# Kernel optimization log

Measured on AMD Instinct MI355X. Metric: run time of the kernel, lower is better.

## Reference

```python
import jax, jax.numpy as jnp
import numpy as np

N = 8192        # nodes
D_IN = 512      # input features
H = 256         # hidden (GAT out_features)
D_OUT = 16      # output classes
K = 16          # num clusters/classes
LRELU_SLOPE = 0.2
MASK_FILL = -9e15
EDGE_P = 0.002  # sparsity of random adjacency


def setup_inputs() -> dict:
    key = jax.random.key(0)
    k1, k2, k3, k4, k5, k6 = jax.random.split(key, 6)
    x = jax.random.normal(k1, (N, D_IN), dtype=jnp.float32)
    # binary adjacency with self loops (module only tests adj > 0; support reused as propagation matrix)
    adj = (jax.random.uniform(k2, (N, N)) < EDGE_P).astype(jnp.float32)
    adj = jnp.maximum(adj, jnp.eye(N, dtype=jnp.float32))
    C_a = jax.random.normal(k3, (K, H), dtype=jnp.float32)
    # learned parameters (xavier-ish scale)
    W = jax.random.normal(k4, (D_IN, H), dtype=jnp.float32) * (1.414 * (2.0 / (D_IN + H)) ** 0.5)
    a = jax.random.normal(k5, (2 * H, 1), dtype=jnp.float32) * (1.414 * (2.0 / (2 * H + 1)) ** 0.5)
    W_gcn = jax.random.normal(k6, (H, D_OUT), dtype=jnp.float32)
    return {"x": x, "adj": adj, "C_a": C_a, "W": W, "a": a, "W_gcn": W_gcn}


def _clust_score(Z, C):
    # score[n,k] = exp(-||Z_n - C_k||) normalized over k (beta = 1)
    d = jnp.sqrt(((Z[:, None, :] - C[None, :, :]) ** 2).sum(-1))  # [N,K]
    s = jnp.exp(-d) + 1e-10
    return s / s.sum(axis=1, keepdims=True)


def reference(x, adj, C_a, W, a, W_gcn):
    h = W.shape[1]
    # --- GAT layer ---
    Wh = x @ W                                   # [N,H]
    Wh1 = Wh @ a[:h, :]                          # [N,1]
    Wh2 = Wh @ a[h:, :]                          # [N,1]
    e = jax.nn.leaky_relu(Wh1 + Wh2.T, LRELU_SLOPE)   # [N,N]
    att = jax.nn.softmax(jnp.where(adj > 0, e, MASK_FILL), axis=1)
    Z_0 = att @ Wh                               # h_prime, [N,H]
    gatoutput = jax.nn.elu(Z_0)
    # --- cluster score on detached Z_0 (update=False path) ---
    score = _clust_score(jax.lax.stop_gradient(Z_0), C_a)
    # --- GCN layer (B_1 = I, so Z_1 = F_1) ---
    F_1 = jax.nn.relu(adj @ (gatoutput @ W_gcn))  # [N,D_OUT]
    output = F_1
    Z_1 = F_1
    return (output, Z_1, Z_0, score)
```

## Files before the change

kernel.cpp:

```cpp
#include <hip/hip_runtime.h>
#include <hip/hip_bf16.h>

#define N_NODES 8192
#define D_IN    512
#define H       256
#define D_OUT   16
#define K_CL    16
#define MAXN    96

#define OUT_OFF 0
#define Z1_OFF  131072
#define Z0_OFF  262144
#define SC_OFF  2359296

typedef unsigned int   u32;
typedef unsigned short u16;
typedef __attribute__((ext_vector_type(8))) short bf16x8;
typedef __attribute__((ext_vector_type(4))) float f32x4;

__device__ __forceinline__ float load_in(const void* p, int bf, size_t idx) {
    if (bf) { u32 w = ((const u16*)p)[idx]; return __uint_as_float(w << 16); }
    return ((const float*)p)[idx];
}
__device__ __forceinline__ void store_out(void* p, int bf, size_t idx, float v) {
    if (bf) ((__hip_bfloat16*)p)[idx] = __float2bfloat16(v);
    else    ((float*)p)[idx] = v;
}
__device__ __forceinline__ int detect_bf(const void* adj) {
    return ((const u32*)adj)[0] != 0x3F800000u;
}
__device__ __forceinline__ float bf2f(u32 h) { return __uint_as_float(h << 16); }

__global__ void k_prep_small(const void* av, const void* C_a, const void* Wgcn,
                             const void* __restrict__ adj,
                             float* a_f, float* Ca_f, float* Wg_f) {
    int bf = detect_bf(adj);
    int i = blockIdx.x * 256 + threadIdx.x;
    if (i < 512)        a_f[i]         = load_in(av,   bf, i);
    else if (i < 4608)  Ca_f[i - 512]  = load_in(C_a,  bf, i - 512);
    else if (i < 8704)  Wg_f[i - 4608] = load_in(Wgcn, bf, i - 4608);
}

__global__ __launch_bounds__(256) void k_prep_wt(
    const void* __restrict__ wraw, const void* __restrict__ adj,
    u16* __restrict__ Wt)
{
    int bf = detect_bf(adj);
    __shared__ float tile[64][65];
    int b = blockIdx.x;
    int k0 = (b >> 2) * 64, h0 = (b & 3) * 64;
    int tid = threadIdx.x;
    int hh = tid & 63, kk = tid >> 6;
    #pragma unroll
    for (int p = 0; p < 16; p++) {
        int k = kk * 16 + p;
        tile[k][hh] = load_in(wraw, bf, (size_t)(k0 + k) * H + h0 + hh);
    }
    __syncthreads();
    int kc = tid & 63, hr = tid >> 6;
    #pragma unroll
    for (int p = 0; p < 16; p++) {
        int h = hr * 16 + p;
        __hip_bfloat16 bb = __float2bfloat16(tile[kc][h]);
        Wt[(size_t)(h0 + h) * D_IN + k0 + kc] = *(u16*)&bb;
    }
}

__global__ __launch_bounds__(256) void k_gemm_wh(
    const void* __restrict__ xraw, const void* __restrict__ wraw,
    const u16* __restrict__ Wt, const void* __restrict__ adj,
    float* __restrict__ Wh, u16* __restrict__ Whb)
{
    int bf = detect_bf(adj);
    __shared__ float xs[32][68];
    __shared__ float ws_[32][68];
    int tid = threadIdx.x;
    int bm = blockIdx.x >> 2, bn = blockIdx.x & 3;
    int m0 = bm * 64, n0 = bn * 64;

    if (bf) {
        int wave = tid >> 6, lane = tid & 63;
        int wr = wave >> 1, wc = wave & 1;
        int r0 = m0 + wr * 32, c0 = n0 + wc * 32;
        int lr = lane & 15, lk = lane >> 4;
        const u16* xp = (const u16*)xraw;
        const u16* a0p = xp + (size_t)(r0 + lr)      * D_IN + lk * 8;
        const u16* a1p = xp + (size_t)(r0 + 16 + lr) * D_IN + lk * 8;
        const u16* b0p = Wt + (size_t)(c0 + lr)      * D_IN + lk * 8;
        const u16* b1p = Wt + (size_t)(c0 + 16 + lr) * D_IN + lk * 8;
        f32x4 acc[2][2] = {};
        #pragma unroll 4
        for (int k0 = 0; k0 < D_IN; k0 += 32) {
            bf16x8 a0 = *(const bf16x8*)(a0p + k0);
            bf16x8 a1 = *(const bf16x8*)(a1p + k0);
            bf16x8 b0 = *(const bf16x8*)(b0p + k0);
            bf16x8 b1 = *(const bf16x8*)(b1p + k0);
            acc[0][0] = __builtin_amdgcn_mfma_f32_16x16x32_bf16(a0, b0, acc[0][0], 0, 0, 0);
            acc[0][1] = __builtin_amdgcn_mfma_f32_16x16x32_bf16(a0, b1, acc[0][1], 0, 0, 0);
            acc[1][0] = __builtin_amdgcn_mfma_f32_16x16x32_bf16(a1, b0, acc[1][0], 0, 0, 0);
            acc[1][1] = __builtin_amdgcn_mfma_f32_16x16x32_bf16(a1, b1, acc[1][1], 0, 0, 0);
        }
        #pragma unroll
        for (int i = 0; i < 2; i++) {
            #pragma unroll
            for (int reg = 0; reg < 4; reg++) {
                int r = r0 + 16 * i + 4 * lk + reg;
                float v0 = acc[i][0][reg], v1 = acc[i][1][reg];
                Wh[(size_t)r * H + c0 + lr]      = v0;
                Wh[(size_t)r * H + c0 + 16 + lr] = v1;
                __hip_bfloat16 h0 = __float2bfloat16(v0), h1 = __float2bfloat16(v1);
                Whb[(size_t)r * H + c0 + lr]      = *(u16*)&h0;
                Whb[(size_t)r * H + c0 + 16 + lr] = *(u16*)&h1;
            }
        }
        return;
    }

    int tx = tid & 15, ty = tid >> 4;
    float acc[4][4] = {};
    for (int k0 = 0; k0 < D_IN; k0 += 32) {
        {
            int r = tid >> 2, kq = (tid & 3) * 8;
            size_t base = (size_t)(m0 + r) * D_IN + k0 + kq;
            float4 f0 = *(const float4*)((const float*)xraw + base);
            float4 f1 = *(const float4*)((const float*)xraw + base + 4);
            xs[kq + 0][r] = f0.x; xs[kq + 1][r] = f0.y;
            xs[kq + 2][r] = f0.z; xs[kq + 3][r] = f0.w;
            xs[kq + 4][r] = f1.x; xs[kq + 5][r] = f1.y;
            xs[kq + 6][r] = f1.z; xs[kq + 7][r] = f1.w;
        }
        {
            int kk = tid >> 3, n8 = (tid & 7) * 8;
            size_t base = (size_t)(k0 + kk) * H + n0 + n8;
            float4 f0 = *(const float4*)((const float*)wraw + base);
            float4 f1 = *(const float4*)((const float*)wraw + base + 4);
            ws_[kk][n8+0]=f0.x; ws_[kk][n8+1]=f0.y; ws_[kk][n8+2]=f0.z; ws_[kk][n8+3]=f0.w;
            ws_[kk][n8+4]=f1.x; ws_[kk][n8+5]=f1.y; ws_[kk][n8+6]=f1.z; ws_[kk][n8+7]=f1.w;
        }
        __syncthreads();
        #pragma unroll
        for (int kk = 0; kk < 32; kk++) {
            float4 a4 = *(const float4*)&xs[kk][ty * 4];
            float4 b4 = *(const float4*)&ws_[kk][tx * 4];
            float a[4] = {a4.x, a4.y, a4.z, a4.w};
            float b[4] = {b4.x, b4.y, b4.z, b4.w};
            #pragma unroll
            for (int i = 0; i < 4; i++)
                #pragma unroll
                for (int j = 0; j < 4; j++)
                    acc[i][j] += a[i] * b[j];
        }
        __syncthreads();
    }
    #pragma unroll
    for (int i = 0; i < 4; i++) {
        float4 o = {acc[i][0], acc[i][1], acc[i][2], acc[i][3]};
        *(float4*)&Wh[(size_t)(m0 + ty*4 + i) * H + n0 + tx*4] = o;
    }
}

__global__ __launch_bounds__(256) void k_wh12(
    const float* __restrict__ Wh, const float* __restrict__ a_f,
    float* __restrict__ Wh1, float* __restrict__ Wh2)
{
    int tid = threadIdx.x;
    int wave = tid >> 6, lane = tid & 63;
    int n = blockIdx.x * 4 + wave;
    float4 v  = *(const float4*)(Wh + (size_t)n * H + lane * 4);
    float4 a1 = *(const float4*)(a_f + lane * 4);
    float4 a2 = *(const float4*)(a_f + H + lane * 4);
    float s1 = v.x*a1.x + v.y*a1.y + v.z*a1.z + v.w*a1.w;
    float s2 = v.x*a2.x + v.y*a2.y + v.z*a2.z + v.w*a2.w;
    #pragma unroll
    for (int off = 32; off; off >>= 1) {
        s1 += __shfl_xor(s1, off);
        s2 += __shfl_xor(s2, off);
    }
    if (lane == 0) { Wh1[n] = s1; Wh2[n] = s2; }
}

__global__ __launch_bounds__(256) void k_gat_row(
    const void* __restrict__ adjraw,
    const float* __restrict__ Wh, const u16* __restrict__ Whb,
    const float* __restrict__ Wh1, const float* __restrict__ Wh2,
    const float* __restrict__ Ca_f, const float* __restrict__ Wg_f,
    float* __restrict__ Gf,
    int* __restrict__ nbr_cnt, u16* __restrict__ nbr_idx,
    void* __restrict__ dout)
{
    const int tid = threadIdx.x;
    const int w = tid >> 6, lane = tid & 63;
    const int n = blockIdx.x * 4 + w;
    const int bf = detect_bf(adjraw);

    __shared__ int   s_cnt[4];
    __shared__ int   s_idx[4][MAXN];
    __shared__ float s_z[4][H];
    __shared__ float s_g[4][H];

    if (lane == 0) s_cnt[w] = 0;

    if (bf) {
        const u16* arow = (const u16*)adjraw + (size_t)n * N_NODES;
        #pragma unroll
        for (int it = 0; it < 16; it++) {
            int base = it * 512 + lane * 8;
            uint4 raw = *(const uint4*)(arow + base);
            if (raw.x | raw.y | raw.z | raw.w) {
                u32 rw[4] = {raw.x, raw.y, raw.z, raw.w};
                #pragma unroll
                for (int q = 0; q < 4; q++)
                    #pragma unroll
                    for (int hh = 0; hh < 2; hh++) {
                        u32 u = (rw[q] >> (16 * hh)) & 0xFFFFu;
                        if (bf2f(u) > 0.f) {
                            int p = atomicAdd(&s_cnt[w], 1);
                            if (p < MAXN) s_idx[w][p] = base + q * 2 + hh;
                        }
                    }
            }
        }
    } else {
        const float* arow = (const float*)adjraw + (size_t)n * N_NODES;
        #pragma unroll
        for (int it = 0; it < 32; it++) {
            int base = it * 256 + lane * 4;
            float4 v = *(const float4*)(arow + base);
            if (v.x + v.y + v.z + v.w > 0.f) {
                float vv[4] = {v.x, v.y, v.z, v.w};
                #pragma unroll
                for (int q = 0; q < 4; q++)
                    if (vv[q] > 0.f) {
                        int p = atomicAdd(&s_cnt[w], 1);
                        if (p < MAXN) s_idx[w][p] = base + q;
                    }
            }
        }
    }
    __syncthreads();
    const int cnt = min(s_cnt[w], MAXN);
    if (lane == 0) nbr_cnt[n] = cnt;
    int i1 = 0, i2 = 0;
    if (lane < cnt)      i1 = s_idx[w][lane];
    if (lane + 64 < cnt) i2 = s_idx[w][lane + 64];
    if (lane < cnt)      nbr_idx[(size_t)n * MAXN + lane]      = (u16)i1;
    if (lane + 64 < cnt) nbr_idx[(size_t)n * MAXN + lane + 64] = (u16)i2;

    const float wh1n = Wh1[n];
    float e1 = -3e38f, e2 = -3e38f;
    if (lane < cnt)      { float v = wh1n + Wh2[i1]; e1 = v > 0.f ? v : 0.2f * v; }
    if (lane + 64 < cnt) { float v = wh1n + Wh2[i2]; e2 = v > 0.f ? v : 0.2f * v; }
    float m = fmaxf(e1, e2);
    #pragma unroll
    for (int off = 32; off; off >>= 1) m = fmaxf(m, __shfl_xor(m, off));
    float x1 = (lane < cnt)      ? expf(e1 - m) : 0.f;
    float x2 = (lane + 64 < cnt) ? expf(e2 - m) : 0.f;
    float ssum = x1 + x2;
    #pragma unroll
    for (int off = 32; off; off >>= 1) ssum += __shfl_xor(ssum, off);
    float inv = 1.f / ssum;
    float at1 = x1 * inv, at2 = x2 * inv;

    const int c4 = lane * 4;
    float az[4] = {0.f, 0.f, 0.f, 0.f};
    if (bf) {
        for (int t = 0; t < cnt; t++) {
            int   it_ = __shfl((t < 64) ? i1 : i2, t & 63);
            float wt_ = __shfl((t < 64) ? at1 : at2, t & 63);
            uint2 r = *(const uint2*)(Whb + (size_t)it_ * H + c4);
            az[0] += wt_ * bf2f(r.x & 0xFFFFu);
            az[1] += wt_ * bf2f(r.x >> 16);
            az[2] += wt_ * bf2f(r.y & 0xFFFFu);
            az[3] += wt_ * bf2f(r.y >> 16);
        }
    } else {
        for (int t = 0; t < cnt; t++) {
            int   it_ = __shfl((t < 64) ? i1 : i2, t & 63);
            float wt_ = __shfl((t < 64) ? at1 : at2, t & 63);
            float4 v = *(const float4*)(Wh + (size_t)it_ * H + c4);
            az[0] += wt_ * v.x; az[1] += wt_ * v.y;
            az[2] += wt_ * v.z; az[3] += wt_ * v.w;
        }
    }
    #pragma unroll
    for (int q = 0; q < 4; q++) {
        float z = az[q];
        store_out(dout, bf, (size_t)Z0_OFF + (size_t)n * H + c4 + q, z);
        s_z[w][c4 + q] = z;
        s_g[w][c4 + q] = z > 0.f ? z : expf(z) - 1.f;
    }
    __syncthreads();

    {
        int k = lane & 15, g = lane >> 4;
        const float* cz = &s_z[w][0];
        const float* ck = Ca_f + (size_t)k * H;
        float d2 = 0.f;
        #pragma unroll 8
        for (int i = 0; i < 64; i++) {
            int ch = g * 64 + ((i + g * 16) & 63);
            float d = cz[ch] - ck[ch];
            d2 += d * d;
        }
        d2 += __shfl_xor(d2, 16);
        d2 += __shfl_xor(d2, 32);
        float sc = expf(-sqrtf(d2)) + 1e-10f;
        float tot = sc;
        tot += __shfl_xor(tot, 1); tot += __shfl_xor(tot, 2);
        tot += __shfl_xor(tot, 4); tot += __shfl_xor(tot, 8);
        if (lane < 16)
            store_out(dout, bf, (size_t)SC_OFF + (size_t)n * K_CL + lane, sc / tot);
    }

    {
        int o = lane & 15, g = lane >> 4;
        const float* cg = &s_g[w][0];
        float p = 0.f;
        #pragma unroll 8
        for (int i = 0; i < 64; i++) {
            int ch = g * 64 + ((i + g * 16) & 63);
            p += cg[ch] * Wg_f[(size_t)ch * D_OUT + o];
        }
        p += __shfl_xor(p, 16);
        p += __shfl_xor(p, 32);
        if (lane < 16) Gf[(size_t)n * D_OUT + lane] = p;
    }
}

__global__ __launch_bounds__(256) void k_f1(
    const int* __restrict__ nbr_cnt, const u16* __restrict__ nbr_idx,
    const float* __restrict__ Gf, const void* __restrict__ adj,
    void* __restrict__ dout)
{
    int tid = threadIdx.x;
    int bf = detect_bf(adj);
    int r = tid >> 4, o = tid & 15;
    int n = blockIdx.x * 16 + r;
    int cnt = nbr_cnt[n];
    const u16* idx = nbr_idx + (size_t)n * MAXN;
    float acc = 0.f;
    int t = 0;
    for (; t + 4 <= cnt; t += 4) {
        int i0 = idx[t], i1 = idx[t+1], i2 = idx[t+2], i3 = idx[t+3];
        float g0 = Gf[(size_t)i0 * D_OUT + o];
        float g1 = Gf[(size_t)i1 * D_OUT + o];
        float g2 = Gf[(size_t)i2 * D_OUT + o];
        float g3 = Gf[(size_t)i3 * D_OUT + o];
        acc += g0; acc += g1; acc += g2; acc += g3;
    }
    for (; t < cnt; t++)
        acc += Gf[(size_t)idx[t] * D_OUT + o];
    acc = fmaxf(acc, 0.f);
    store_out(dout, bf, (size_t)OUT_OFF + (size_t)n * D_OUT + o, acc);
    store_out(dout, bf, (size_t)Z1_OFF  + (size_t)n * D_OUT + o, acc);
}

extern "C" void kernel_launch(void* const* d_in, const int* in_sizes, int n_in,
                              void* d_out, int out_size, void* d_ws, size_t ws_size,
                              hipStream_t stream) {
    const void* x    = d_in[0];
    const void* adj  = d_in[1];
    const void* C_a  = d_in[2];
    const void* W    = d_in[3];
    const void* av   = d_in[4];
    const void* Wgcn = d_in[5];

    char* wsp = (char*)d_ws;
    float* Wh   = (float*)wsp;                 wsp += (size_t)N_NODES * H * 4;
    u16*   Whb  = (u16*)wsp;                   wsp += (size_t)N_NODES * H * 2;
    float* Wh1  = (float*)wsp;                 wsp += (size_t)N_NODES * 4;
    float* Wh2  = (float*)wsp;                 wsp += (size_t)N_NODES * 4;
    float* Gf   = (float*)wsp;                 wsp += (size_t)N_NODES * D_OUT * 4;
    int*   ncnt = (int*)wsp;                   wsp += (size_t)N_NODES * 4;
    u16*   nidx = (u16*)wsp;                   wsp += (size_t)N_NODES * MAXN * 2;
    float* a_f  = (float*)wsp;                 wsp += 2 * H * 4;
    float* Ca_f = (float*)wsp;                 wsp += (size_t)K_CL * H * 4;
    float* Wg_f = (float*)wsp;                 wsp += (size_t)H * D_OUT * 4;
    u16*   Wt   = (u16*)wsp;                   wsp += (size_t)H * D_IN * 2;

    k_prep_small<<<34, 256, 0, stream>>>(av, C_a, Wgcn, adj, a_f, Ca_f, Wg_f);
    k_prep_wt   <<<32, 256, 0, stream>>>(W, adj, Wt);
    k_gemm_wh   <<<512, 256, 0, stream>>>(x, W, Wt, adj, Wh, Whb);
    k_wh12      <<<N_NODES / 4, 256, 0, stream>>>(Wh, a_f, Wh1, Wh2);
    k_gat_row   <<<N_NODES / 4, 256, 0, stream>>>(adj, Wh, Whb, Wh1, Wh2, Ca_f, Wg_f,
                                                  Gf, ncnt, nidx, d_out);
    k_f1        <<<N_NODES / 16, 256, 0, stream>>>(ncnt, nidx, Gf, adj, d_out);
}
```

Measured before the change: 494.9 us.

## Batch adjacency row loads, unroll neighbor gather, merge prep kernels

Merges the two small prep kernels into one launch. In the GAT row kernel, each wave now issues eight 16-byte adjacency loads before scanning them, which raises memory-level parallelism on the dominant N×N adjacency read. It also tests nonzero as raw bits instead of as a float compare. The neighbor aggregation is unrolled by four so several gathers are in flight at once. The cost is higher register pressure, and the bit test treats a negative or -0 value as an edge, which the float compare did not.

After: 469.6 us. 5.1% less time.

```diff
diff --git a/kernel.cpp b/kernel.cpp
--- a/kernel.cpp
+++ b/kernel.cpp
@@ -31,25 +31,22 @@
 }
 __device__ __forceinline__ float bf2f(u32 h) { return __uint_as_float(h << 16); }
 
-__global__ void k_prep_small(const void* av, const void* C_a, const void* Wgcn,
-                             const void* __restrict__ adj,
-                             float* a_f, float* Ca_f, float* Wg_f) {
-    int bf = detect_bf(adj);
-    int i = blockIdx.x * 256 + threadIdx.x;
-    if (i < 512)        a_f[i]         = load_in(av,   bf, i);
-    else if (i < 4608)  Ca_f[i - 512]  = load_in(C_a,  bf, i - 512);
-    else if (i < 8704)  Wg_f[i - 4608] = load_in(Wgcn, bf, i - 4608);
-}
-
-__global__ __launch_bounds__(256) void k_prep_wt(
-    const void* __restrict__ wraw, const void* __restrict__ adj,
-    u16* __restrict__ Wt)
+__global__ __launch_bounds__(256) void k_prep(
+    const void* __restrict__ wraw, const void* av, const void* C_a, const void* Wgcn,
+    const void* __restrict__ adj,
+    u16* __restrict__ Wt, float* a_f, float* Ca_f, float* Wg_f)
 {
     int bf = detect_bf(adj);
+    int b = blockIdx.x, tid = threadIdx.x;
+    if (b >= 32) {
+        int i = (b - 32) * 256 + tid;
+        if (i < 512)        a_f[i]         = load_in(av,   bf, i);
+        else if (i < 4608)  Ca_f[i - 512]  = load_in(C_a,  bf, i - 512);
+        else if (i < 8704)  Wg_f[i - 4608] = load_in(Wgcn, bf, i - 4608);
+        return;
+    }
     __shared__ float tile[64][65];
-    int b = blockIdx.x;
     int k0 = (b >> 2) * 64, h0 = (b & 3) * 64;
-    int tid = threadIdx.x;
     int hh = tid & 63, kk = tid >> 6;
     #pragma unroll
     for (int p = 0; p < 16; p++) {
@@ -203,37 +200,49 @@
     if (bf) {
         const u16* arow = (const u16*)adjraw + (size_t)n * N_NODES;
         #pragma unroll
-        for (int it = 0; it < 16; it++) {
-            int base = it * 512 + lane * 8;
-            uint4 raw = *(const uint4*)(arow + base);
-            if (raw.x | raw.y | raw.z | raw.w) {
-                u32 rw[4] = {raw.x, raw.y, raw.z, raw.w};
+        for (int rnd = 0; rnd < 2; rnd++) {
+            uint4 r[8];
+            #pragma unroll
+            for (int it = 0; it < 8; it++)
+                r[it] = *(const uint4*)(arow + rnd * 4096 + it * 512 + lane * 8);
+            #pragma unroll
+            for (int it = 0; it < 8; it++) {
+                u32 w4[4] = {r[it].x, r[it].y, r[it].z, r[it].w};
+                int base = rnd * 4096 + it * 512 + lane * 8;
                 #pragma unroll
-                for (int q = 0; q < 4; q++)
-                    #pragma unroll
-                    for (int hh = 0; hh < 2; hh++) {
-                        u32 u = (rw[q] >> (16 * hh)) & 0xFFFFu;
-                        if (bf2f(u) > 0.f) {
+                for (int q = 0; q < 4; q++) {
+                    if (w4[q]) {
+                        if (w4[q] & 0xFFFFu) {
                             int p = atomicAdd(&s_cnt[w], 1);
-                            if (p < MAXN) s_idx[w][p] = base + q * 2 + hh;
+                            if (p < MAXN) s_idx[w][p] = base + q * 2;
+                        }
+                        if (w4[q] >> 16) {
+                            int p = atomicAdd(&s_cnt[w], 1);
+                            if (p < MAXN) s_idx[w][p] = base + q * 2 + 1;
                         }
                     }
+                }
             }
         }
     } else {
-        const float* arow = (const float*)adjraw + (size_t)n * N_NODES;
+        const u32* arow = (const u32*)adjraw + (size_t)n * N_NODES;
         #pragma unroll
-        for (int it = 0; it < 32; it++) {
-            int base = it * 256 + lane * 4;
-            float4 v = *(const float4*)(arow + base);
-            if (v.x + v.y + v.z + v.w > 0.f) {
-                float vv[4] = {v.x, v.y, v.z, v.w};
+        for (int rnd = 0; rnd < 4; rnd++) {
+            uint4 r[8];
+            #pragma unroll
+            for (int it = 0; it < 8; it++)
+                r[it] = *(const uint4*)(arow + rnd * 2048 + it * 256 + lane * 4);
+            #pragma unroll
+            for (int it = 0; it < 8; it++) {
+                u32 w4[4] = {r[it].x, r[it].y, r[it].z, r[it].w};
+                int base = rnd * 2048 + it * 256 + lane * 4;
                 #pragma unroll
-                for (int q = 0; q < 4; q++)
-                    if (vv[q] > 0.f) {
+                for (int q = 0; q < 4; q++) {
+                    if (w4[q]) {
                         int p = atomicAdd(&s_cnt[w], 1);
                         if (p < MAXN) s_idx[w][p] = base + q;
                     }
+                }
             }
         }
     }
@@ -264,7 +273,28 @@
     const int c4 = lane * 4;
     float az[4] = {0.f, 0.f, 0.f, 0.f};
     if (bf) {
-        for (int t = 0; t < cnt; t++) {
+        int t = 0;
+        for (; t + 4 <= cnt; t += 4) {
+            int ja[4]; float wa[4];
+            #pragma unroll
+            for (int u = 0; u < 4; u++) {
+                int tt = t + u;
+                ja[u] = __shfl((tt < 64) ? i1 : i2, tt & 63);
+                wa[u] = __shfl((tt < 64) ? at1 : at2, tt & 63);
+            }
+            uint2 rr[4];
+            #pragma unroll
+            for (int u = 0; u < 4; u++)
+                rr[u] = *(const uint2*)(Whb + (size_t)ja[u] * H + c4);
+            #pragma unroll
+            for (int u = 0; u < 4; u++) {
+                az[0] += wa[u] * bf2f(rr[u].x & 0xFFFFu);
+                az[1] += wa[u] * bf2f(rr[u].x >> 16);
+                az[2] += wa[u] * bf2f(rr[u].y & 0xFFFFu);
+                az[3] += wa[u] * bf2f(rr[u].y >> 16);
+            }
+        }
+        for (; t < cnt; t++) {
             int   it_ = __shfl((t < 64) ? i1 : i2, t & 63);
             float wt_ = __shfl((t < 64) ? at1 : at2, t & 63);
             uint2 r = *(const uint2*)(Whb + (size_t)it_ * H + c4);
@@ -274,7 +304,26 @@
             az[3] += wt_ * bf2f(r.y >> 16);
         }
     } else {
-        for (int t = 0; t < cnt; t++) {
+        int t = 0;
+        for (; t + 4 <= cnt; t += 4) {
+            int ja[4]; float wa[4];
+            #pragma unroll
+            for (int u = 0; u < 4; u++) {
+                int tt = t + u;
+                ja[u] = __shfl((tt < 64) ? i1 : i2, tt & 63);
+                wa[u] = __shfl((tt < 64) ? at1 : at2, tt & 63);
+            }
+            float4 rr[4];
+            #pragma unroll
+            for (int u = 0; u < 4; u++)
+                rr[u] = *(const float4*)(Wh + (size_t)ja[u] * H + c4);
+            #pragma unroll
+            for (int u = 0; u < 4; u++) {
+                az[0] += wa[u] * rr[u].x; az[1] += wa[u] * rr[u].y;
+                az[2] += wa[u] * rr[u].z; az[3] += wa[u] * rr[u].w;
+            }
+        }
+        for (; t < cnt; t++) {
             int   it_ = __shfl((t < 64) ? i1 : i2, t & 63);
             float wt_ = __shfl((t < 64) ? at1 : at2, t & 63);
             float4 v = *(const float4*)(Wh + (size_t)it_ * H + c4);
@@ -378,11 +427,10 @@
     float* Wg_f = (float*)wsp;                 wsp += (size_t)H * D_OUT * 4;
     u16*   Wt   = (u16*)wsp;                   wsp += (size_t)H * D_IN * 2;
 
-    k_prep_small<<<34, 256, 0, stream>>>(av, C_a, Wgcn, adj, a_f, Ca_f, Wg_f);
-    k_prep_wt   <<<32, 256, 0, stream>>>(W, adj, Wt);
-    k_gemm_wh   <<<512, 256, 0, stream>>>(x, W, Wt, adj, Wh, Whb);
-    k_wh12      <<<N_NODES / 4, 256, 0, stream>>>(Wh, a_f, Wh1, Wh2);
-    k_gat_row   <<<N_NODES / 4, 256, 0, stream>>>(adj, Wh, Whb, Wh1, Wh2, Ca_f, Wg_f,
-                                                  Gf, ncnt, nidx, d_out);
-    k_f1        <<<N_NODES / 16, 256, 0, stream>>>(ncnt, nidx, Gf, adj, d_out);
-}
+    k_prep    <<<66, 256, 0, stream>>>(W, av, C_a, Wgcn, adj, Wt, a_f, Ca_f, Wg_f);
+    k_gemm_wh <<<512, 256, 0, stream>>>(x, W, Wt, adj, Wh, Whb);
+    k_wh12    <<<N_NODES / 4, 256, 0, stream>>>(Wh, a_f, Wh1, Wh2);
+    k_gat_row <<<N_NODES / 4, 256, 0, stream>>>(adj, Wh, Whb, Wh1, Wh2, Ca_f, Wg_f,
+                                                Gf, ncnt, nidx, d_out);
+    k_f1      <<<N_NODES / 16, 256, 0, stream>>>(ncnt, nidx, Gf, adj, d_out);
+}
```
